# Kernel optimization log

Measured on AMD Instinct MI355X. Metric: run time of the kernel, lower is better.

## Reference

```python
import jax, jax.numpy as jnp
import numpy as np

B, H, W, C, WS, SHIFT, NH = 64, 14, 14, 1024, 7, 3, 32
HD = C // NH
SCALE = HD ** -0.5

def _rel_index():
    coords = np.stack(np.meshgrid(np.arange(WS), np.arange(WS), indexing='ij'))  # [2,ws,ws]
    flat = coords.reshape(2, -1)
    rel = (flat[:, :, None] - flat[:, None, :]).transpose(1, 2, 0)  # [49,49,2]
    rel[:, :, 0] += WS - 1
    rel[:, :, 1] += WS - 1
    rel[:, :, 0] *= 2 * WS - 1
    return jnp.asarray(rel.sum(-1))  # [49,49] int

REL_IDX = _rel_index()

def _shift_mask():
    m = np.zeros((H, W), np.float32)
    cnt = 0
    for hs in (slice(0, -WS), slice(-WS, -SHIFT), slice(-SHIFT, None)):
        for ws_ in (slice(0, -WS), slice(-WS, -SHIFT), slice(-SHIFT, None)):
            m[hs, ws_] = cnt
            cnt += 1
    mw = m.reshape(H // WS, WS, W // WS, WS).transpose(0, 2, 1, 3).reshape(-1, WS * WS)
    diff = mw[:, None, :] - mw[:, :, None]
    return jnp.asarray(np.where(diff != 0, -100.0, 0.0).astype(np.float32))  # [nW,49,49]

ATTN_MASK = _shift_mask()

def layernorm(x, g, b, eps=1e-5):
    mu = x.mean(-1, keepdims=True)
    var = ((x - mu) ** 2).mean(-1, keepdims=True)
    return (x - mu) * jax.lax.rsqrt(var + eps) * g + b

def window_partition(x):  # [B,H,W,C] -> [B*nW, 49, C]
    x = x.reshape(B, H // WS, WS, W // WS, WS, C)
    return x.transpose(0, 1, 3, 2, 4, 5).reshape(-1, WS * WS, C)

def window_reverse(x):  # [B*nW, 49, C] -> [B,H,W,C]
    x = x.reshape(B, H // WS, W // WS, WS, WS, C)
    return x.transpose(0, 1, 3, 2, 4, 5).reshape(B, H, W, C)

def swin_block(x, p, shift):
    (ln1_g, ln1_b, qkv_w, qkv_b, rpb, proj_w, proj_b,
     ln2_g, ln2_b, fc1_w, fc1_b, fc2_w, fc2_b) = p
    h = layernorm(x, ln1_g, ln1_b).reshape(B, H, W, C)
    if shift:
        h = jnp.roll(h, (-SHIFT, -SHIFT), axis=(1, 2))
    hw = window_partition(h)                              # [Bn,49,C]
    qkv = hw @ qkv_w + qkv_b                              # [Bn,49,3C]
    q, k, v = qkv.reshape(-1, WS * WS, 3, NH, HD).transpose(2, 0, 3, 1, 4)  # each [Bn,NH,49,HD]
    attn = jnp.einsum('bhqd,bhkd->bhqk', q * SCALE, k)    # [Bn,NH,49,49]
    attn = attn + rpb[REL_IDX].transpose(2, 0, 1)[None]   # fused rel-pos bias
    if shift:
        nW = ATTN_MASK.shape[0]
        attn = attn.reshape(B, nW, NH, WS * WS, WS * WS) + ATTN_MASK[None, :, None]
        attn = attn.reshape(-1, NH, WS * WS, WS * WS)
    attn = jax.nn.softmax(attn, axis=-1)
    o = jnp.einsum('bhqk,bhkd->bhqd', attn, v).transpose(0, 2, 1, 3).reshape(-1, WS * WS, C)
    o = o @ proj_w + proj_b
    o = window_reverse(o)
    if shift:
        o = jnp.roll(o, (SHIFT, SHIFT), axis=(1, 2))
    x = x + o.reshape(B, H * W, C)
    h2 = layernorm(x, ln2_g, ln2_b)
    return x + jax.nn.gelu(h2 @ fc1_w + fc1_b, approximate=False) @ fc2_w + fc2_b

def setup_inputs() -> dict:
    key = jax.random.key(0)
    ks = iter(jax.random.split(key, 64))
    def rnd(shape, s=0.02):
        return jax.random.normal(next(ks), shape, jnp.float32) * s
    inp = {'x': jax.random.normal(next(ks), (B, H * W, C), jnp.float32)}
    for i in range(2):
        inp[f'b{i}_ln1_g'] = jnp.ones((C,), jnp.float32)
        inp[f'b{i}_ln1_b'] = jnp.zeros((C,), jnp.float32)
        inp[f'b{i}_qkv_w'] = rnd((C, 3 * C))
        inp[f'b{i}_qkv_b'] = jnp.zeros((3 * C,), jnp.float32)
        inp[f'b{i}_rpb'] = rnd(((2 * WS - 1) ** 2, NH))
        inp[f'b{i}_proj_w'] = rnd((C, C))
        inp[f'b{i}_proj_b'] = jnp.zeros((C,), jnp.float32)
        inp[f'b{i}_ln2_g'] = jnp.ones((C,), jnp.float32)
        inp[f'b{i}_ln2_b'] = jnp.zeros((C,), jnp.float32)
        inp[f'b{i}_fc1_w'] = rnd((C, 4 * C))
        inp[f'b{i}_fc1_b'] = jnp.zeros((4 * C,), jnp.float32)
        inp[f'b{i}_fc2_w'] = rnd((4 * C, C))
        inp[f'b{i}_fc2_b'] = jnp.zeros((C,), jnp.float32)
    inp['h_ln_g'] = jnp.ones((C,), jnp.float32)
    inp['h_ln_b'] = jnp.zeros((C,), jnp.float32)
    inp['h_w1'] = rnd((C, 512)); inp['h_b1'] = jnp.zeros((512,), jnp.float32)
    inp['h_w2'] = rnd((512, 128)); inp['h_b2'] = jnp.zeros((128,), jnp.float32)
    inp['h_w3'] = rnd((128, 2)); inp['h_b3'] = jnp.zeros((2,), jnp.float32)
    return inp

def reference(x,
              b0_ln1_g, b0_ln1_b, b0_qkv_w, b0_qkv_b, b0_rpb, b0_proj_w, b0_proj_b,
              b0_ln2_g, b0_ln2_b, b0_fc1_w, b0_fc1_b, b0_fc2_w, b0_fc2_b,
              b1_ln1_g, b1_ln1_b, b1_qkv_w, b1_qkv_b, b1_rpb, b1_proj_w, b1_proj_b,
              b1_ln2_g, b1_ln2_b, b1_fc1_w, b1_fc1_b, b1_fc2_w, b1_fc2_b,
              h_ln_g, h_ln_b, h_w1, h_b1, h_w2, h_b2, h_w3, h_b3):
    p0 = (b0_ln1_g, b0_ln1_b, b0_qkv_w, b0_qkv_b, b0_rpb, b0_proj_w, b0_proj_b,
          b0_ln2_g, b0_ln2_b, b0_fc1_w, b0_fc1_b, b0_fc2_w, b0_fc2_b)
    p1 = (b1_ln1_g, b1_ln1_b, b1_qkv_w, b1_qkv_b, b1_rpb, b1_proj_w, b1_proj_b,
          b1_ln2_g, b1_ln2_b, b1_fc1_w, b1_fc1_b, b1_fc2_w, b1_fc2_b)
    x = swin_block(x, p0, shift=False)
    x = swin_block(x, p1, shift=True)
    pooled = x.mean(axis=1)  # global avg pool -> [B, C]
    h = layernorm(pooled, h_ln_g, h_ln_b)
    h = jax.nn.gelu(h @ h_w1 + h_b1, approximate=False)  # dropout is identity (eval)
    h = jax.nn.gelu(h @ h_w2 + h_b2, approximate=False)
    return h @ h_w3 + h_b3  # [B, num_classes]
```

## Files before the change

### kernel.cpp

```cpp
#include <hip/hip_runtime.h>
#include <hip/hip_bf16.h>
#include <hip/hip_fp16.h>
#include <math.h>

#define BB 64
#define CC 1024
#define NH 32
#define NTOK (BB * 14 * 14)
#define SCALE 0.17677669529663687f

typedef __attribute__((ext_vector_type(8))) short short8;
typedef __attribute__((ext_vector_type(8))) unsigned short us8;
typedef __attribute__((ext_vector_type(4))) float f32x4;

__device__ __align__(16) float  g_X  [(size_t)NTOK * CC];
__device__ __align__(16) float  g_QKV[(size_t)NTOK * 3072];
__device__ __align__(16) unsigned short g_B[(size_t)NTOK * CC];
__device__ __align__(16) unsigned short g_C[(size_t)NTOK * 4096];
__device__ __align__(16) unsigned short g_Wq[(size_t)2*3072*1024];
__device__ __align__(16) unsigned short g_Wp[(size_t)2*1024*1024];
__device__ __align__(16) unsigned short g_W1[(size_t)2*4096*1024];
__device__ __align__(16) unsigned short g_W2[(size_t)2*1024*4096];
__device__ __align__(16) float g_H0[64 * CC];
__device__ __align__(16) float g_H1[64 * 512];
__device__ __align__(16) float g_H2[64 * 128];

__device__ __forceinline__ float gelu_f(float x) {
    return 0.5f * x * (1.0f + erff(x * 0.70710678118654752f));
}

__device__ __forceinline__ unsigned short f16_bits(float v) {
    _Float16 hh = (_Float16)v;
    return *(unsigned short*)&hh;
}

__device__ __forceinline__ int win_to_xrow(int r, int shifted) {
    int bn = r / 49, t = r - bn * 49;
    int b = bn >> 2, w = bn & 3;
    int wh = w >> 1, ww_ = w & 1;
    int th = t / 7, tw = t - th * 7;
    int gh = wh * 7 + th, gw = ww_ * 7 + tw;
    if (shifted) { gh = gh + 3; if (gh >= 14) gh -= 14; gw = gw + 3; if (gw >= 14) gw -= 14; }
    return b * 196 + gh * 14 + gw;
}

__device__ __forceinline__ void gload_lds16(const void* g, void* l) {
    __builtin_amdgcn_global_load_lds(
        (const __attribute__((address_space(1))) unsigned int*)g,
        (__attribute__((address_space(3))) unsigned int*)l, 16, 0, 0);
}

__global__ __launch_bounds__(256) void convw_kernel(const float* __restrict__ W,
    unsigned short* __restrict__ Wh, int K, int N)
{
    __shared__ float t[32][33];
    int n0 = blockIdx.x * 32, k0 = blockIdx.y * 32;
    int tx = threadIdx.x & 31, ty = threadIdx.x >> 5;
    #pragma unroll
    for (int i = 0; i < 4; ++i)
        t[ty + 8 * i][tx] = W[(size_t)(k0 + ty + 8 * i) * N + n0 + tx];
    __syncthreads();
    #pragma unroll
    for (int i = 0; i < 4; ++i) {
        int n = ty + 8 * i;
        Wh[(size_t)(n0 + n) * K + k0 + tx] = f16_bits(t[tx][n]);
    }
}

__global__ __launch_bounds__(256) void ln_kernel(const float* __restrict__ X,
    const float* __restrict__ g, const float* __restrict__ bta,
    unsigned short* __restrict__ outh, int shifted, int partition)
{
    int token = blockIdx.x * 4 + (threadIdx.x >> 6);
    int lane = threadIdx.x & 63;
    int xrow = partition ? win_to_xrow(token, shifted) : token;
    const float4* src = (const float4*)(X + (size_t)xrow * CC);
    float4 v[4];
    float s = 0.f;
    #pragma unroll
    for (int w = 0; w < 4; ++w) {
        v[w] = src[w * 64 + lane];
        s += v[w].x + v[w].y + v[w].z + v[w].w;
    }
    #pragma unroll
    for (int o = 32; o; o >>= 1) s += __shfl_xor(s, o);
    float mean = s * (1.0f / CC);
    float ss = 0.f;
    #pragma unroll
    for (int w = 0; w < 4; ++w) {
        float d0 = v[w].x - mean, d1 = v[w].y - mean, d2 = v[w].z - mean, d3 = v[w].w - mean;
        ss += d0 * d0 + d1 * d1 + d2 * d2 + d3 * d3;
    }
    #pragma unroll
    for (int o = 32; o; o >>= 1) ss += __shfl_xor(ss, o);
    float inv = 1.0f / sqrtf(ss * (1.0f / CC) + 1e-5f);
    #pragma unroll
    for (int w = 0; w < 4; ++w) {
        int c4 = w * 64 + lane;
        float4 gv = *(const float4*)(g + c4 * 4);
        float4 bv = *(const float4*)(bta + c4 * 4);
        ushort4 uo;
        uo.x = f16_bits((v[w].x - mean) * inv * gv.x + bv.x);
        uo.y = f16_bits((v[w].y - mean) * inv * gv.y + bv.y);
        uo.z = f16_bits((v[w].z - mean) * inv * gv.z + bv.z);
        uo.w = f16_bits((v[w].w - mean) * inv * gv.w + bv.w);
        *(ushort4*)(outh + (size_t)token * CC + c4 * 4) = uo;
    }
}

template<int EPI>
__global__ __launch_bounds__(256, 2) void gemm_mfma(
    const unsigned short* __restrict__ A, const unsigned short* __restrict__ W,
    const float* __restrict__ bias,
    float* __restrict__ outf, unsigned short* __restrict__ outh,
    int N, int K, int shifted, int NR, int GC)
{
    __shared__ unsigned short sm[EPI == 1 ? 16896 : 16384];
    const int tid = threadIdx.x;
    const int wave = tid >> 6, lane = tid & 63;
    const int wr = wave >> 1, wc = wave & 1;
    const int nb = gridDim.x;
    const int wg = (blockIdx.x & 7) * (nb >> 3) + (blockIdx.x >> 3);
    const int gsz = GC * NR;
    const int grp = wg / gsz;
    const int rem = wg - grp * gsz;
    const int by = rem / GC;
    const int bx = grp * GC + (rem - by * GC);
    const int row0 = by * 128, col0 = bx * 128;
    const int rsel = lane & 15;

    f32x4 acc[4][4] = {};

    const int srow = tid >> 3, sslot = tid & 7;

    for (int k0 = 0; k0 < K; k0 += 64) {
        #pragma unroll
        for (int i = 0; i < 8; ++i) {
            const int t = i >> 2;
            const int sub = i & 3;
            const int row = sub * 32 + srow;
            const int c = sslot ^ (row & 7);
            const unsigned short* gp = (t == 0) ? A : W;
            const int rb = (t == 0) ? row0 : col0;
            gload_lds16(gp + (size_t)(rb + row) * K + k0 + c * 8,
                        &sm[t * 8192 + sub * 2048 + tid * 8]);
        }
        __syncthreads();

        #pragma unroll
        for (int kk = 0; kk < 2; ++kk) {
            const int kc8 = kk * 4 + (lane >> 4);
            short8 fa[4], fw[4];
            #pragma unroll
            for (int m = 0; m < 4; ++m) {
                int ra = wr * 64 + m * 16 + rsel;
                fa[m] = *(const short8*)&sm[ra * 64 + ((kc8 ^ (ra & 7)) * 8)];
                int rw = wc * 64 + m * 16 + rsel;
                fw[m] = *(const short8*)&sm[8192 + rw * 64 + ((kc8 ^ (rw & 7)) * 8)];
            }
            #pragma unroll
            for (int m = 0; m < 4; ++m)
                #pragma unroll
                for (int n = 0; n < 4; ++n)
                    acc[m][n] = __builtin_amdgcn_mfma_f32_16x16x32_f16(fa[m], fw[n], acc[m][n], 0, 0, 0);
        }
        __syncthreads();
    }

    const int jrow = lane >> 4;
    if (EPI == 1) {
        #pragma unroll
        for (int n = 0; n < 4; ++n) {
            int cl = wc * 64 + n * 16 + rsel;
            float bv = bias[col0 + cl];
            #pragma unroll
            for (int m = 0; m < 4; ++m)
                #pragma unroll
                for (int j = 0; j < 4; ++j) {
                    int rl = wr * 64 + m * 16 + jrow * 4 + j;
                    sm[rl * 132 + cl] = f16_bits(gelu_f(acc[m][n][j] + bv));
                }
        }
        __syncthreads();
        const int r = tid >> 1, cb = (tid & 1) * 64;
        unsigned short* dst = outh + (size_t)(row0 + r) * N + col0 + cb;
        const unsigned short* src = &sm[r * 132 + cb];
        #pragma unroll
        for (int i = 0; i < 8; ++i)
            *(us8*)(dst + i * 8) = *(const us8*)(src + i * 8);
    } else {
        #pragma unroll
        for (int n = 0; n < 4; ++n) {
            int c = col0 + wc * 64 + n * 16 + rsel;
            float bv = bias[c];
            #pragma unroll
            for (int m = 0; m < 4; ++m) {
                #pragma unroll
                for (int j = 0; j < 4; ++j) {
                    int r = row0 + wr * 64 + m * 16 + jrow * 4 + j;
                    float v = acc[m][n][j] + bv;
                    if (EPI == 0) {
                        outf[(size_t)r * N + c] = v;
                    } else if (EPI == 2) {
                        outf[(size_t)win_to_xrow(r, shifted) * CC + c] += v;
                    } else {
                        outf[(size_t)r * CC + c] += v;
                    }
                }
            }
        }
    }
}

__global__ __launch_bounds__(256) void attn_kernel(const float* __restrict__ qkv,
    unsigned short* __restrict__ oh, const float* __restrict__ rpb, int shifted)
{
    int blk = blockIdx.x;
    int bn = blk >> 3;
    int hg = blk & 7;
    int wv = threadIdx.x >> 6;
    int lane = threadIdx.x & 63;
    int h = hg * 4 + wv;

    __shared__ float ks[4][49][32], vs[4][49][32];

    for (int idx = lane; idx < 49 * 32; idx += 64) {
        int t = idx >> 5, d = idx & 31;
        const float* p = qkv + (size_t)(bn * 49 + t) * 3072 + h * 32 + d;
        ks[wv][t][d] = p[1024];
        vs[wv][t][d] = p[2048];
    }
    __syncthreads();

    if (lane < 49) {
        const int i = lane;
        const int ih = i / 7, iw = i - ih * 7;
        const int w = bn & 3, wh = w >> 1, ww_ = w & 1;
        const int gh = wh * 7 + ih, gw = ww_ * 7 + iw;
        const int li = (gh < 7 ? 0 : (gh < 11 ? 1 : 2)) * 3 + (gw < 7 ? 0 : (gw < 11 ? 1 : 2));

        float qreg[32];
        const float* qp = qkv + (size_t)(bn * 49 + i) * 3072 + h * 32;
        #pragma unroll
        for (int d4 = 0; d4 < 8; ++d4) {
            float4 qv = *(const float4*)(qp + d4 * 4);
            qreg[d4 * 4 + 0] = qv.x * SCALE;
            qreg[d4 * 4 + 1] = qv.y * SCALE;
            qreg[d4 * 4 + 2] = qv.z * SCALE;
            qreg[d4 * 4 + 3] = qv.w * SCALE;
        }

        float p[49];
        float mx = -1e30f;
        #pragma unroll
        for (int j = 0; j < 49; ++j) {
            const int jh = j / 7, jw = j - jh * 7;
            float dot = 0.f;
            #pragma unroll
            for (int d = 0; d < 32; ++d) dot = fmaf(qreg[d], ks[wv][j][d], dot);
            const int ridx = (ih - jh + 6) * 13 + (iw - jw + 6);
            float val = dot + rpb[ridx * 32 + h];
            if (shifted) {
                const int gjh = wh * 7 + jh, gjw = ww_ * 7 + jw;
                const int lj = (gjh < 7 ? 0 : (gjh < 11 ? 1 : 2)) * 3 +
                               (gjw < 7 ? 0 : (gjw < 11 ? 1 : 2));
                if (li != lj) val -= 100.0f;
            }
            p[j] = val;
            mx = fmaxf(mx, val);
        }
        float denom = 0.f;
        #pragma unroll
        for (int j = 0; j < 49; ++j) {
            p[j] = expf(p[j] - mx);
            denom += p[j];
        }
        const float rd = 1.0f / denom;

        unsigned short* orow = oh + (size_t)(bn * 49 + i) * CC + h * 32;
        #pragma unroll 4
        for (int d = 0; d < 32; ++d) {
            float acc = 0.f;
            #pragma unroll
            for (int j = 0; j < 49; ++j) acc = fmaf(p[j], vs[wv][j][d], acc);
            orow[d] = f16_bits(acc * rd);
        }
    }
}

__global__ __launch_bounds__(256) void pool_ln_kernel(const float* __restrict__ X,
    const float* __restrict__ g, const float* __restrict__ bta, float* __restrict__ out)
{
    int b = blockIdx.x, tid = threadIdx.x;
    int lane = tid & 63, wid = tid >> 6;
    const float* base = X + (size_t)b * 196 * CC + tid * 4;
    float a0 = 0, a1 = 0, a2 = 0, a3 = 0;
    for (int t = 0; t < 196; ++t) {
        float4 v = *(const float4*)(base + (size_t)t * CC);
        a0 += v.x; a1 += v.y; a2 += v.z; a3 += v.w;
    }
    const float inv196 = 1.0f / 196.0f;
    float p0 = a0 * inv196, p1 = a1 * inv196, p2 = a2 * inv196, p3 = a3 * inv196;
    float s = p0 + p1 + p2 + p3;
    #pragma unroll
    for (int o = 32; o; o >>= 1) s += __shfl_xor(s, o);
    __shared__ float sred[4], ssred[4];
    if (lane == 0) sred[wid] = s;
    __syncthreads();
    float mean = (sred[0] + sred[1] + sred[2] + sred[3]) * (1.0f / CC);
    float d0 = p0 - mean, d1 = p1 - mean, d2 = p2 - mean, d3 = p3 - mean;
    float ss = d0 * d0 + d1 * d1 + d2 * d2 + d3 * d3;
    #pragma unroll
    for (int o = 32; o; o >>= 1) ss += __shfl_xor(ss, o);
    if (lane == 0) ssred[wid] = ss;
    __syncthreads();
    float var = (ssred[0] + ssred[1] + ssred[2] + ssred[3]) * (1.0f / CC);
    float inv = 1.0f / sqrtf(var + 1e-5f);
    float4 gv = *(const float4*)(g + tid * 4);
    float4 bv = *(const float4*)(bta + tid * 4);
    float4 o4;
    o4.x = d0 * inv * gv.x + bv.x;
    o4.y = d1 * inv * gv.y + bv.y;
    o4.z = d2 * inv * gv.z + bv.z;
    o4.w = d3 * inv * gv.w + bv.w;
    *(float4*)(out + (size_t)b * CC + tid * 4) = o4;
}

__global__ __launch_bounds__(256) void head_rowgemm(const float* __restrict__ A,
    const float* __restrict__ W, const float* __restrict__ bias,
    float* __restrict__ out, int K, int N, int act)
{
    __shared__ float As[1024];
    int r = blockIdx.x, tid = threadIdx.x;
    for (int k = tid; k < K; k += 256) As[k] = A[(size_t)r * K + k];
    __syncthreads();
    for (int c = tid; c < N; c += 256) {
        float s0 = 0.f, s1 = 0.f;
        for (int k = 0; k < K; k += 2) {
            s0 = fmaf(As[k],     W[(size_t)k * N + c],       s0);
            s1 = fmaf(As[k + 1], W[(size_t)(k + 1) * N + c], s1);
        }
        float s = s0 + s1 + bias[c];
        out[(size_t)r * N + c] = act ? gelu_f(s) : s;
    }
}

extern "C" void kernel_launch(void* const* d_in, const int* in_sizes, int n_in,
                              void* d_out, int out_size, void* d_ws, size_t ws_size,
                              hipStream_t stream) {
    const float* x = (const float*)d_in[0];
    auto P = [&](int i) { return (const float*)d_in[i]; };

    float *X, *QKV, *H0, *H1, *H2;
    unsigned short *B, *C, *Wq, *Wp, *W1, *W2;
    { void* p;
      hipGetSymbolAddress(&p, HIP_SYMBOL(g_X));   X   = (float*)p;
      hipGetSymbolAddress(&p, HIP_SYMBOL(g_QKV)); QKV = (float*)p;
      hipGetSymbolAddress(&p, HIP_SYMBOL(g_B));   B   = (unsigned short*)p;
      hipGetSymbolAddress(&p, HIP_SYMBOL(g_C));   C   = (unsigned short*)p;
      hipGetSymbolAddress(&p, HIP_SYMBOL(g_Wq));  Wq  = (unsigned short*)p;
      hipGetSymbolAddress(&p, HIP_SYMBOL(g_Wp));  Wp  = (unsigned short*)p;
      hipGetSymbolAddress(&p, HIP_SYMBOL(g_W1));  W1  = (unsigned short*)p;
      hipGetSymbolAddress(&p, HIP_SYMBOL(g_W2));  W2  = (unsigned short*)p;
      hipGetSymbolAddress(&p, HIP_SYMBOL(g_H0));  H0 = (float*)p;
      hipGetSymbolAddress(&p, HIP_SYMBOL(g_H1));  H1 = (float*)p;
      hipGetSymbolAddress(&p, HIP_SYMBOL(g_H2));  H2 = (float*)p;
    }

    hipMemcpyAsync(X, x, (size_t)NTOK * CC * sizeof(float),
                   hipMemcpyDeviceToDevice, stream);

    for (int blk = 0; blk < 2; ++blk) {
        int base = 1 + blk * 13;
        convw_kernel<<<dim3(3072/32, 1024/32), 256, 0, stream>>>(
            P(base + 2), Wq + (size_t)blk*3072*1024, 1024, 3072);
        convw_kernel<<<dim3(1024/32, 1024/32), 256, 0, stream>>>(
            P(base + 5), Wp + (size_t)blk*1024*1024, 1024, 1024);
        convw_kernel<<<dim3(4096/32, 1024/32), 256, 0, stream>>>(
            P(base + 9), W1 + (size_t)blk*4096*1024, 1024, 4096);
        convw_kernel<<<dim3(1024/32, 4096/32), 256, 0, stream>>>(
            P(base + 11), W2 + (size_t)blk*1024*4096, 4096, 1024);
    }

    for (int blk = 0; blk < 2; ++blk) {
        int base = 1 + blk * 13;
        const float *ln1g = P(base + 0), *ln1b = P(base + 1);
        const float *qkvb = P(base + 3);
        const float *rpb  = P(base + 4);
        const float *projb = P(base + 6);
        const float *ln2g = P(base + 7), *ln2b = P(base + 8);
        const float *fc1b = P(base + 10);
        const float *fc2b = P(base + 12);
        int shifted = blk;
        const unsigned short* wq = Wq + (size_t)blk*3072*1024;
        const unsigned short* wp = Wp + (size_t)blk*1024*1024;
        const unsigned short* w1 = W1 + (size_t)blk*4096*1024;
        const unsigned short* w2 = W2 + (size_t)blk*1024*4096;

        ln_kernel<<<NTOK / 4, 256, 0, stream>>>(X, ln1g, ln1b, B, shifted, 1);
        gemm_mfma<0><<<2352, 256, 0, stream>>>(
            B, wq, qkvb, QKV, nullptr, 3072, 1024, 0, 98, 8);
        attn_kernel<<<256 * 8, 256, 0, stream>>>(QKV, B, rpb, shifted);
        gemm_mfma<2><<<784, 256, 0, stream>>>(
            B, wp, projb, X, nullptr, 1024, 1024, shifted, 98, 8);
        ln_kernel<<<NTOK / 4, 256, 0, stream>>>(X, ln2g, ln2b, B, 0, 0);
        gemm_mfma<1><<<3136, 256, 0, stream>>>(
            B, w1, fc1b, nullptr, C, 4096, 1024, 0, 98, 8);
        gemm_mfma<3><<<784, 256, 0, stream>>>(
            C, w2, fc2b, X, nullptr, 1024, 4096, 0, 98, 2);
    }

    pool_ln_kernel<<<64, 256, 0, stream>>>(X, P(27), P(28), H0);
    head_rowgemm<<<64, 256, 0, stream>>>(H0, P(29), P(30), H1, 1024, 512, 1);
    head_rowgemm<<<64, 256, 0, stream>>>(H1, P(31), P(32), H2, 512, 128, 1);
    head_rowgemm<<<64, 256, 0, stream>>>(H2, P(33), P(34), (float*)d_out, 128, 2, 0);
}
```

Baseline: 1.579 ms.

## Double-buffer GEMM LDS tiles and stage residual-add epilogue through shared memory

Splits the GEMM's LDS into two stages so the next K-tile's global-to-LDS loads are issued before the MFMA work on the current tile, leaving one barrier per iteration instead of two. The residual-add epilogues (proj and fc2) now write results into LDS in two halves and then do coalesced float4 read-modify-writes to X, replacing scattered per-element accesses. The fc2 launch's tile-group column count also changes from 2 to 8. Doubling LDS to 64 KB per block may limit occupancy against the requested 2 blocks per CU.

```diff
diff --git a/kernel.cpp b/kernel.cpp
--- a/kernel.cpp
+++ b/kernel.cpp
@@ -115,7 +115,7 @@
     float* __restrict__ outf, unsigned short* __restrict__ outh,
     int N, int K, int shifted, int NR, int GC)
 {
-    __shared__ unsigned short sm[EPI == 1 ? 16896 : 16384];
+    __shared__ unsigned short sm[32768];
     const int tid = threadIdx.x;
     const int wave = tid >> 6, lane = tid & 63;
     const int wr = wave >> 1, wc = wave & 1;
@@ -133,7 +133,7 @@
 
     const int srow = tid >> 3, sslot = tid & 7;
 
-    for (int k0 = 0; k0 < K; k0 += 64) {
+    auto STAGE = [&](int bufSel, int k0) {
         #pragma unroll
         for (int i = 0; i < 8; ++i) {
             const int t = i >> 2;
@@ -143,10 +143,20 @@
             const unsigned short* gp = (t == 0) ? A : W;
             const int rb = (t == 0) ? row0 : col0;
             gload_lds16(gp + (size_t)(rb + row) * K + k0 + c * 8,
-                        &sm[t * 8192 + sub * 2048 + tid * 8]);
-        }
-        __syncthreads();
-
+                        &sm[bufSel * 16384 + t * 8192 + sub * 2048 + tid * 8]);
+        }
+    };
+
+    const int nt = K >> 6;
+    int cur = 0;
+    STAGE(0, 0);
+    asm volatile("s_waitcnt vmcnt(0)" ::: "memory");
+    __builtin_amdgcn_sched_barrier(0);
+    __builtin_amdgcn_s_barrier();
+
+    for (int t = 0; t < nt; ++t) {
+        if (t + 1 < nt) STAGE(cur ^ 1, (t + 1) << 6);
+        const int bb = cur * 16384;
         #pragma unroll
         for (int kk = 0; kk < 2; ++kk) {
             const int kc8 = kk * 4 + (lane >> 4);
@@ -154,9 +164,9 @@
             #pragma unroll
             for (int m = 0; m < 4; ++m) {
                 int ra = wr * 64 + m * 16 + rsel;
-                fa[m] = *(const short8*)&sm[ra * 64 + ((kc8 ^ (ra & 7)) * 8)];
+                fa[m] = *(const short8*)&sm[bb + ra * 64 + ((kc8 ^ (ra & 7)) * 8)];
                 int rw = wc * 64 + m * 16 + rsel;
-                fw[m] = *(const short8*)&sm[8192 + rw * 64 + ((kc8 ^ (rw & 7)) * 8)];
+                fw[m] = *(const short8*)&sm[bb + 8192 + rw * 64 + ((kc8 ^ (rw & 7)) * 8)];
             }
             #pragma unroll
             for (int m = 0; m < 4; ++m)
@@ -164,11 +174,27 @@
                 for (int n = 0; n < 4; ++n)
                     acc[m][n] = __builtin_amdgcn_mfma_f32_16x16x32_f16(fa[m], fw[n], acc[m][n], 0, 0, 0);
         }
-        __syncthreads();
+        asm volatile("s_waitcnt vmcnt(0)" ::: "memory");
+        __builtin_amdgcn_sched_barrier(0);
+        __builtin_amdgcn_s_barrier();
+        cur ^= 1;
     }
 
     const int jrow = lane >> 4;
-    if (EPI == 1) {
+    if (EPI == 0) {
+        #pragma unroll
+        for (int n = 0; n < 4; ++n) {
+            int c = col0 + wc * 64 + n * 16 + rsel;
+            float bv = bias[c];
+            #pragma unroll
+            for (int m = 0; m < 4; ++m)
+                #pragma unroll
+                for (int j = 0; j < 4; ++j) {
+                    int r = row0 + wr * 64 + m * 16 + jrow * 4 + j;
+                    outf[(size_t)r * N + c] = acc[m][n][j] + bv;
+                }
+        }
+    } else if (EPI == 1) {
         #pragma unroll
         for (int n = 0; n < 4; ++n) {
             int cl = wc * 64 + n * 16 + rsel;
@@ -189,24 +215,37 @@
         for (int i = 0; i < 8; ++i)
             *(us8*)(dst + i * 8) = *(const us8*)(src + i * 8);
     } else {
-        #pragma unroll
-        for (int n = 0; n < 4; ++n) {
-            int c = col0 + wc * 64 + n * 16 + rsel;
-            float bv = bias[c];
-            #pragma unroll
-            for (int m = 0; m < 4; ++m) {
+        float* smf = (float*)sm;
+        const int rr = tid >> 2;
+        const int cc4 = (tid & 3) * 32;
+        #pragma unroll
+        for (int half = 0; half < 2; ++half) {
+            __syncthreads();
+            if (wr == half) {
                 #pragma unroll
-                for (int j = 0; j < 4; ++j) {
-                    int r = row0 + wr * 64 + m * 16 + jrow * 4 + j;
-                    float v = acc[m][n][j] + bv;
-                    if (EPI == 0) {
-                        outf[(size_t)r * N + c] = v;
-                    } else if (EPI == 2) {
-                        outf[(size_t)win_to_xrow(r, shifted) * CC + c] += v;
-                    } else {
-                        outf[(size_t)r * CC + c] += v;
-                    }
+                for (int n = 0; n < 4; ++n) {
+                    const int cl = wc * 64 + n * 16 + rsel;
+                    const float bv = bias[col0 + cl];
+                    #pragma unroll
+                    for (int m = 0; m < 4; ++m)
+                        #pragma unroll
+                        for (int j = 0; j < 4; ++j)
+                            smf[(m * 16 + jrow * 4 + j) * 130 + cl] = acc[m][n][j] + bv;
                 }
+            }
+            __syncthreads();
+            const int gr = row0 + half * 64 + rr;
+            const int orow = (EPI == 2) ? win_to_xrow(gr, shifted) : gr;
+            float* dst = outf + (size_t)orow * CC + col0 + cc4;
+            const float* srcl = &smf[rr * 130 + cc4];
+            #pragma unroll
+            for (int i = 0; i < 8; ++i) {
+                float4 xv = *(float4*)(dst + i * 4);
+                xv.x += srcl[i * 4 + 0];
+                xv.y += srcl[i * 4 + 1];
+                xv.z += srcl[i * 4 + 2];
+                xv.w += srcl[i * 4 + 3];
+                *(float4*)(dst + i * 4) = xv;
             }
         }
     }
@@ -407,7 +446,7 @@
         gemm_mfma<1><<<3136, 256, 0, stream>>>(
             B, w1, fc1b, nullptr, C, 4096, 1024, 0, 98, 8);
         gemm_mfma<3><<<784, 256, 0, stream>>>(
-            C, w2, fc2b, X, nullptr, 1024, 4096, 0, 98, 2);
+            C, w2, fc2b, X, nullptr, 1024, 4096, 0, 98, 8);
     }
 
     pool_ln_kernel<<<64, 256, 0, stream>>>(X, P(27), P(28), H0);
```

Measured after the change: 1.680 ms. 1.06x slower.
